# Kernel tuning notes

Hardware: AMD Instinct MI355X
Metric: run time of the kernel (lower is better)

The kernel has to match this reference:

```python
import jax, jax.numpy as jnp
import numpy as np

H = 4096          # hidden_size
M = 4096          # num tokens
BLK = 128         # fp8 quant group/block size
EPS = 1e-6
FP8_MAX = 448.0   # float8_e4m3fn max


def fp8_round(x):
    # round-trip through fp8 e4m3 to emulate FP8 storage
    return x.astype(jnp.float8_e4m3fn).astype(jnp.float32)


def rms_norm(x, w, eps=EPS):
    var = jnp.mean(x * x, axis=-1, keepdims=True)
    return x * jax.lax.rsqrt(var + eps) * w


def block_fp8_linear(x, w, wscale):
    # per-token group-128 activation quant + 128x128 block-scaled fp8 GEMM
    m, k = x.shape
    kb = k // BLK
    nb = w.shape[1] // BLK
    xr = x.reshape(m, kb, BLK)
    amax = jnp.max(jnp.abs(xr), axis=-1)                      # [m, kb]
    s = jnp.maximum(amax, 1e-12) / FP8_MAX                    # group scales
    q = fp8_round(xr / s[..., None])                          # fp8 values
    xdq = (q * s[..., None]).reshape(m, k)                    # dequant acts
    # dequantize weight blockwise: w already fp8-valued floats
    wdq = (w.reshape(kb, BLK, nb, BLK) * wscale[:, None, :, None]).reshape(k, nb * BLK)
    return xdq @ wdq


def setup_inputs() -> dict:
    key = jax.random.key(0)
    ks = jax.random.split(key, 8)
    x = jax.random.normal(ks[0], (M, H), dtype=jnp.float32)
    sb = H // BLK
    d = {"x": x}
    for i in range(3):
        w = fp8_round(jax.random.uniform(ks[1 + i], (H, H), dtype=jnp.float32)).T
        d[f"w{i}"] = w
        d[f"ws{i}"] = jax.random.uniform(ks[4 + i], (sb, sb), dtype=jnp.float32)
    for i in range(4):
        d[f"nw{i}"] = jnp.ones((H,), dtype=jnp.float32)
    return d


def reference(x, w0, ws0, w1, ws1, w2, ws2, nw0, nw1, nw2, nw3):
    x = jax.nn.relu(x)
    resid = x
    y = rms_norm(x, nw0)
    x2 = block_fp8_linear(y, w0, ws0)
    resid = x2 + resid
    y2 = rms_norm(resid, nw1)
    x3 = block_fp8_linear(y2, w1, ws1)
    resid = x3 + resid
    y3 = rms_norm(resid, nw2)
    x4 = block_fp8_linear(y3, w2, ws2)
    resid = x4 + resid
    y4 = rms_norm(resid, nw3)
    return y4
```

## Files before the change

kernel.cpp:

```cpp
#include <hip/hip_runtime.h>
#include <stdint.h>

#define H 4096

typedef float v4f __attribute__((ext_vector_type(4)));
typedef long long i64;
typedef long long v2l __attribute__((ext_vector_type(2)));

__device__ __forceinline__ void gload16(const uint8_t* g, uint8_t* l) {
  __builtin_amdgcn_global_load_lds(
      (const __attribute__((address_space(1))) uint8_t*)g,
      (__attribute__((address_space(3))) uint8_t*)l, 16, 0, 0);
}

__device__ __forceinline__ int permpos(int kg) {
  const int kb = kg >> 7, b = kg & 127;
  const int ks = b >> 5, q = (b >> 3) & 3, j = b & 7;
  return kb * 128 + q * 32 + ks * 8 + j;
}

__global__ __launch_bounds__(256) void conv_w_kernel(
    const float* __restrict__ w0, const float* __restrict__ w1,
    const float* __restrict__ w2, uint8_t* __restrict__ o0,
    uint8_t* __restrict__ o1, uint8_t* __restrict__ o2) {
  const float* w = (blockIdx.z == 0) ? w0 : (blockIdx.z == 1 ? w1 : w2);
  uint8_t* o = (blockIdx.z == 0) ? o0 : (blockIdx.z == 1 ? o1 : o2);
  __shared__ uint8_t t[64][68];
  const int tid = threadIdx.x;
  const int k0 = blockIdx.y * 64, n0 = blockIdx.x * 64;
  const int rr = tid >> 4, cc = (tid & 15) * 4;
#pragma unroll
  for (int j = 0; j < 4; ++j) {
    const int r = rr + j * 16;
    v4f f = *(const v4f*)(w + (size_t)(k0 + r) * H + n0 + cc);
    unsigned p = __builtin_amdgcn_cvt_pk_fp8_f32(f.x, f.y, 0, false);
    p = __builtin_amdgcn_cvt_pk_fp8_f32(f.z, f.w, p, true);
    t[cc + 0][r] = p & 0xff;
    t[cc + 1][r] = (p >> 8) & 0xff;
    t[cc + 2][r] = (p >> 16) & 0xff;
    t[cc + 3][r] = p >> 24;
  }
  __syncthreads();
#pragma unroll
  for (int j = 0; j < 4; ++j) {
    const int n = rr + j * 16;
    unsigned p = (unsigned)t[n][cc] | ((unsigned)t[n][cc + 1] << 8) |
                 ((unsigned)t[n][cc + 2] << 16) |
                 ((unsigned)t[n][cc + 3] << 24);
    *(unsigned*)(o + (size_t)(n0 + n) * H + permpos(k0 + cc)) = p;
  }
}

__global__ __launch_bounds__(256) void quant_kernel(
    const float* in, const float* __restrict__ nw, uint8_t* __restrict__ q,
    float* __restrict__ sxT, const int relu) {
  const int row = blockIdx.x, tid = threadIdx.x;
  const v4f* rp = (const v4f*)(in + (size_t)row * H);
  v4f v[4];
  float ss = 0.f;
#pragma unroll
  for (int j = 0; j < 4; ++j) {
    v4f x = rp[j * 256 + tid];
    if (relu) {
      x.x = fmaxf(x.x, 0.f); x.y = fmaxf(x.y, 0.f);
      x.z = fmaxf(x.z, 0.f); x.w = fmaxf(x.w, 0.f);
    }
    v[j] = x;
    ss += x.x * x.x + x.y * x.y + x.z * x.z + x.w * x.w;
  }
#pragma unroll
  for (int o = 32; o > 0; o >>= 1) ss += __shfl_down(ss, o);
  __shared__ float red[4];
  if ((tid & 63) == 0) red[tid >> 6] = ss;
  __syncthreads();
  ss = red[0] + red[1] + red[2] + red[3];
  const float rinv = 1.f / sqrtf(ss * (1.f / H) + 1e-6f);
#pragma unroll
  for (int j = 0; j < 4; ++j) {
    v4f nv = ((const v4f*)nw)[j * 256 + tid];
    v4f y;
    y.x = v[j].x * rinv * nv.x;
    y.y = v[j].y * rinv * nv.y;
    y.z = v[j].z * rinv * nv.z;
    y.w = v[j].w * rinv * nv.w;
    float am = fmaxf(fmaxf(fabsf(y.x), fabsf(y.y)), fmaxf(fabsf(y.z), fabsf(y.w)));
#pragma unroll
    for (int o = 16; o > 0; o >>= 1) am = fmaxf(am, __shfl_xor(am, o, 32));
    const float s = fmaxf(am, 1e-12f) / 448.f;
    unsigned p = __builtin_amdgcn_cvt_pk_fp8_f32(y.x / s, y.y / s, 0, false);
    p = __builtin_amdgcn_cvt_pk_fp8_f32(y.z / s, y.w / s, p, true);
    const int col = (j * 256 + tid) * 4;
    *(unsigned*)(q + (size_t)row * H + permpos(col)) = p;
    if ((tid & 31) == 0)
      sxT[(size_t)(j * 8 + (tid >> 5)) * 4096 + row] = s;
  }
}

__global__ __launch_bounds__(256) void norm_kernel(float* io,
                                                   const float* __restrict__ nw) {
  const int row = blockIdx.x, tid = threadIdx.x;
  v4f* rp = (v4f*)(io + (size_t)row * H);
  v4f v[4];
  float ss = 0.f;
#pragma unroll
  for (int j = 0; j < 4; ++j) {
    v4f x = rp[j * 256 + tid];
    v[j] = x;
    ss += x.x * x.x + x.y * x.y + x.z * x.z + x.w * x.w;
  }
#pragma unroll
  for (int o = 32; o > 0; o >>= 1) ss += __shfl_down(ss, o);
  __shared__ float red[4];
  if ((tid & 63) == 0) red[tid >> 6] = ss;
  __syncthreads();
  ss = red[0] + red[1] + red[2] + red[3];
  const float rinv = 1.f / sqrtf(ss * (1.f / H) + 1e-6f);
#pragma unroll
  for (int j = 0; j < 4; ++j) {
    v4f nv = ((const v4f*)nw)[j * 256 + tid];
    v4f y;
    y.x = v[j].x * rinv * nv.x;
    y.y = v[j].y * rinv * nv.y;
    y.z = v[j].z * rinv * nv.z;
    y.w = v[j].w * rinv * nv.w;
    rp[j * 256 + tid] = y;
  }
}

__global__ __launch_bounds__(256, 4) void gemm_kernel(
    const uint8_t* __restrict__ qa,
    const float* __restrict__ sxT,
    const uint8_t* __restrict__ wt,
    const float* __restrict__ ws,
    const float* resid, float* outp, const int relu) {
  __shared__ __attribute__((aligned(16))) uint8_t sA[16384];
  __shared__ __attribute__((aligned(16))) uint8_t sB[16384];
  __shared__ __attribute__((aligned(16))) float scb[128];
  __shared__ float ws_s[32];

  const int tid = threadIdx.x;
  const int n0 = blockIdx.x * 128, m0 = blockIdx.y * 128;
  if (tid < 32) ws_s[tid] = ws[tid * 32 + blockIdx.x];

  const int wv = tid >> 6, lane = tid & 63;
  const int quad = lane >> 4, l16 = lane & 15;
  const int wm = wv >> 1, wn = wv & 1;

  const int swc = (tid & 7) ^ ((tid >> 3) & 7);
  const uint8_t* gA = qa + (size_t)(m0 + (tid >> 3)) * H + swc * 16;
  const uint8_t* gB = wt + (size_t)(n0 + (tid >> 3)) * H + swc * 16;
  const uint8_t* gS = (const uint8_t*)sxT + (size_t)m0 * 4 + lane * 16;
  uint8_t* lA = sA + wv * 1024;
  uint8_t* lB = sB + wv * 1024;

  int offp[2];
#pragma unroll
  for (int ksp = 0; ksp < 2; ++ksp)
    offp[ksp] = (((quad * 2 + ksp) ^ (l16 & 7)) << 4);
  const int arow = (wm * 64 + l16) * 128;
  const int brow = (wn * 64 + l16) * 128;
  const int scoff = wm * 64 + quad * 4;

  const v4f zf = {0.f, 0.f, 0.f, 0.f};
  v4f acc[4][4];
#pragma unroll
  for (int i = 0; i < 4; ++i)
#pragma unroll
    for (int j = 0; j < 4; ++j) acc[i][j] = zf;

  for (int kb = 0; kb < 32; ++kb) {
#pragma unroll
    for (int i = 0; i < 4; ++i) {
      gload16(gA + (size_t)i * (32 * H), lA + i * 4096);
      gload16(gB + (size_t)i * (32 * H), lB + i * 4096);
    }
    if (wv == 0 && lane < 32) gload16(gS + (size_t)kb * 16384, (uint8_t*)scb);
    gA += 128;
    gB += 128;
    __syncthreads();

    const float wsk = ws_s[kb];
    v2l bf[4][2];
#pragma unroll
    for (int tc = 0; tc < 4; ++tc)
#pragma unroll
      for (int ksp = 0; ksp < 2; ++ksp)
        bf[tc][ksp] = *(const v2l*)(sB + brow + tc * 2048 + offp[ksp]);

#pragma unroll
    for (int tr = 0; tr < 4; ++tr) {
      const v2l a0 = *(const v2l*)(sA + arow + tr * 2048 + offp[0]);
      const v2l a1 = *(const v2l*)(sA + arow + tr * 2048 + offp[1]);
      const v4f s4 = *(const v4f*)(scb + scoff + tr * 16) * wsk;
#pragma unroll
      for (int tc = 0; tc < 4; ++tc) {
        v4f p = __builtin_amdgcn_mfma_f32_16x16x32_fp8_fp8(a0.x, bf[tc][0].x, zf, 0, 0, 0);
        p = __builtin_amdgcn_mfma_f32_16x16x32_fp8_fp8(a0.y, bf[tc][0].y, p, 0, 0, 0);
        p = __builtin_amdgcn_mfma_f32_16x16x32_fp8_fp8(a1.x, bf[tc][1].x, p, 0, 0, 0);
        p = __builtin_amdgcn_mfma_f32_16x16x32_fp8_fp8(a1.y, bf[tc][1].y, p, 0, 0, 0);
        acc[tr][tc] += p * s4;
      }
    }
    __syncthreads();
  }

  const int mB = m0 + wm * 64 + quad * 4;
  const int nB = n0 + wn * 64 + l16;
#pragma unroll
  for (int tr = 0; tr < 4; ++tr) {
#pragma unroll
    for (int r = 0; r < 4; ++r) {
      const size_t rowOff = (size_t)(mB + tr * 16 + r) * H;
#pragma unroll
      for (int tc = 0; tc < 4; ++tc) {
        const size_t idx = rowOff + nB + tc * 16;
        float rv = resid[idx];
        if (relu) rv = fmaxf(rv, 0.f);
        outp[idx] = acc[tr][tc][r] + rv;
      }
    }
  }
}

extern "C" void kernel_launch(void* const* d_in, const int* in_sizes, int n_in,
                              void* d_out, int out_size, void* d_ws, size_t ws_size,
                              hipStream_t stream) {
  const float* x   = (const float*)d_in[0];
  const float* w0  = (const float*)d_in[1];
  const float* ws0 = (const float*)d_in[2];
  const float* w1  = (const float*)d_in[3];
  const float* ws1 = (const float*)d_in[4];
  const float* w2  = (const float*)d_in[5];
  const float* ws2 = (const float*)d_in[6];
  const float* nw0 = (const float*)d_in[7];
  const float* nw1 = (const float*)d_in[8];
  const float* nw2 = (const float*)d_in[9];
  const float* nw3 = (const float*)d_in[10];
  float* R = (float*)d_out;

  uint8_t* base = (uint8_t*)d_ws;
  uint8_t* wq0 = base;
  uint8_t* wq1 = base + ((size_t)16 << 20);
  uint8_t* wq2 = base + ((size_t)32 << 20);
  uint8_t* qa  = base + ((size_t)48 << 20);
  float* sa    = (float*)(base + ((size_t)64 << 20));

  conv_w_kernel<<<dim3(64, 64, 3), 256, 0, stream>>>(w0, w1, w2, wq0, wq1, wq2);

  quant_kernel<<<4096, 256, 0, stream>>>(x, nw0, qa, sa, 1);
  gemm_kernel<<<dim3(32, 32), 256, 0, stream>>>(qa, sa, wq0, ws0, x, R, 1);

  quant_kernel<<<4096, 256, 0, stream>>>(R, nw1, qa, sa, 0);
  gemm_kernel<<<dim3(32, 32), 256, 0, stream>>>(qa, sa, wq1, ws1, R, R, 0);

  quant_kernel<<<4096, 256, 0, stream>>>(R, nw2, qa, sa, 0);
  gemm_kernel<<<dim3(32, 32), 256, 0, stream>>>(qa, sa, wq2, ws2, R, R, 0);

  norm_kernel<<<4096, 256, 0, stream>>>(R, nw3);
}
```

Measured before the change: 686.7 us.

## Enlarge GEMM tile to 256x256 with double-buffered LDS prefetch

The block-scaled FP8 GEMM moves from 128x128 tiles with 256 threads to 256x256 tiles with 512 threads. LDS is double-buffered, and the next K-block's global-to-LDS loads are issued in four phases interleaved with the MFMA work. Block IDs are remapped so neighbouring blocks share A/B panels in L2, and s_setprio is raised around the MFMA sections. The aim is to cut per-tile global traffic and hide load latency behind compute. In exchange there are 256 blocks over 256 CUs (about one wave), much more LDS (about 130KB) and more accumulator registers.

After: 771.2 us. +12.3%, slower.

```diff
diff --git a/kernel.cpp b/kernel.cpp
--- a/kernel.cpp
+++ b/kernel.cpp
@@ -127,87 +127,120 @@
   }
 }
 
-__global__ __launch_bounds__(256, 4) void gemm_kernel(
+__global__ __launch_bounds__(512, 2) void gemm_kernel(
     const uint8_t* __restrict__ qa,
     const float* __restrict__ sxT,
     const uint8_t* __restrict__ wt,
     const float* __restrict__ ws,
     const float* resid, float* outp, const int relu) {
-  __shared__ __attribute__((aligned(16))) uint8_t sA[16384];
-  __shared__ __attribute__((aligned(16))) uint8_t sB[16384];
-  __shared__ __attribute__((aligned(16))) float scb[128];
-  __shared__ float ws_s[32];
+  __shared__ __attribute__((aligned(16))) uint8_t sA[2][32768];
+  __shared__ __attribute__((aligned(16))) uint8_t sB[2][32768];
+  __shared__ __attribute__((aligned(16))) float scb[2][256];
+  __shared__ float ws_s[64];
 
   const int tid = threadIdx.x;
-  const int n0 = blockIdx.x * 128, m0 = blockIdx.y * 128;
-  if (tid < 32) ws_s[tid] = ws[tid * 32 + blockIdx.x];
-
-  const int wv = tid >> 6, lane = tid & 63;
+
+  const int lid = blockIdx.y * 16 + blockIdx.x;
+  const int nl = (lid & 7) * 32 + (lid >> 3);
+  const int m0 = (nl >> 4) * 256, n0 = (nl & 15) * 256;
+
+  const int w = tid >> 6, lane = tid & 63;
   const int quad = lane >> 4, l16 = lane & 15;
-  const int wm = wv >> 1, wn = wv & 1;
-
-  const int swc = (tid & 7) ^ ((tid >> 3) & 7);
-  const uint8_t* gA = qa + (size_t)(m0 + (tid >> 3)) * H + swc * 16;
-  const uint8_t* gB = wt + (size_t)(n0 + (tid >> 3)) * H + swc * 16;
+  const int wm = w >> 2, wn = w & 3;
+  const int whalf = wn >> 1;
+
+  if (tid < 64) ws_s[tid] = ws[(tid >> 1) * 32 + (n0 >> 7) + (tid & 1)];
+
+  const int sw = (tid & 7) ^ ((tid >> 3) & 7);
+  const uint8_t* gA = qa + (size_t)(m0 + (tid >> 3)) * H + sw * 16;
+  const uint8_t* gB = wt + (size_t)(n0 + (tid >> 3)) * H + sw * 16;
   const uint8_t* gS = (const uint8_t*)sxT + (size_t)m0 * 4 + lane * 16;
-  uint8_t* lA = sA + wv * 1024;
-  uint8_t* lB = sB + wv * 1024;
+  const int ldst = w * 1024;
+
+#pragma unroll
+  for (int i = 0; i < 4; ++i) {
+    gload16(gA + (size_t)i * (64 * H), sA[0] + i * 8192 + ldst);
+    gload16(gB + (size_t)i * (64 * H), sB[0] + i * 8192 + ldst);
+  }
+  if (w == 0) gload16(gS, (uint8_t*)scb[0]);
 
   int offp[2];
 #pragma unroll
   for (int ksp = 0; ksp < 2; ++ksp)
     offp[ksp] = (((quad * 2 + ksp) ^ (l16 & 7)) << 4);
-  const int arow = (wm * 64 + l16) * 128;
-  const int brow = (wn * 64 + l16) * 128;
-  const int scoff = wm * 64 + quad * 4;
 
   const v4f zf = {0.f, 0.f, 0.f, 0.f};
-  v4f acc[4][4];
-#pragma unroll
-  for (int i = 0; i < 4; ++i)
+  v4f acc[8][4];
+#pragma unroll
+  for (int i = 0; i < 8; ++i)
 #pragma unroll
     for (int j = 0; j < 4; ++j) acc[i][j] = zf;
 
+  __syncthreads();
+
   for (int kb = 0; kb < 32; ++kb) {
-#pragma unroll
-    for (int i = 0; i < 4; ++i) {
-      gload16(gA + (size_t)i * (32 * H), lA + i * 4096);
-      gload16(gB + (size_t)i * (32 * H), lB + i * 4096);
+    const int cur = kb & 1, nxt = cur ^ 1;
+    const uint8_t* Ab = sA[cur];
+    const uint8_t* Bb = sB[cur];
+    const float* sc = scb[cur];
+    const float wsk = ws_s[kb * 2 + whalf];
+    const bool pf = (kb < 31);
+    v2l bf[4][2];
+
+#pragma unroll
+    for (int p = 0; p < 4; ++p) {
+      if (p == 0) {
+#pragma unroll
+        for (int tc = 0; tc < 4; ++tc)
+#pragma unroll
+          for (int ksp = 0; ksp < 2; ++ksp)
+            bf[tc][ksp] =
+                *(const v2l*)(Bb + (wn * 64 + tc * 16 + l16) * 128 + offp[ksp]);
+      }
+      v2l a[2][2];
+      v4f s4[2];
+#pragma unroll
+      for (int t = 0; t < 2; ++t) {
+        const int row = wm * 128 + (p * 2 + t) * 16 + l16;
+        a[t][0] = *(const v2l*)(Ab + row * 128 + offp[0]);
+        a[t][1] = *(const v2l*)(Ab + row * 128 + offp[1]);
+        s4[t] = *(const v4f*)(sc + wm * 128 + (p * 2 + t) * 16 + quad * 4);
+      }
+      if (pf) {
+        gload16(gA + 128 + (size_t)p * (64 * H), sA[nxt] + p * 8192 + ldst);
+        gload16(gB + 128 + (size_t)p * (64 * H), sB[nxt] + p * 8192 + ldst);
+        if (p == 0 && w == 0) gload16(gS + 16384, (uint8_t*)scb[nxt]);
+      }
+      __builtin_amdgcn_s_barrier();
+      asm volatile("s_waitcnt lgkmcnt(0)" ::: "memory");
+      __builtin_amdgcn_sched_barrier(0);
+      __builtin_amdgcn_s_setprio(1);
+#pragma unroll
+      for (int t = 0; t < 2; ++t) {
+        const int tr = p * 2 + t;
+        const v4f sv = s4[t] * wsk;
+#pragma unroll
+        for (int tc = 0; tc < 4; ++tc) {
+          v4f pr = __builtin_amdgcn_mfma_f32_16x16x32_fp8_fp8(a[t][0].x, bf[tc][0].x, zf, 0, 0, 0);
+          pr = __builtin_amdgcn_mfma_f32_16x16x32_fp8_fp8(a[t][0].y, bf[tc][0].y, pr, 0, 0, 0);
+          pr = __builtin_amdgcn_mfma_f32_16x16x32_fp8_fp8(a[t][1].x, bf[tc][1].x, pr, 0, 0, 0);
+          pr = __builtin_amdgcn_mfma_f32_16x16x32_fp8_fp8(a[t][1].y, bf[tc][1].y, pr, 0, 0, 0);
+          acc[tr][tc] += pr * sv;
+        }
+      }
+      __builtin_amdgcn_s_setprio(0);
+      if (p == 3) asm volatile("s_waitcnt vmcnt(0)" ::: "memory");
+      __builtin_amdgcn_s_barrier();
     }
-    if (wv == 0 && lane < 32) gload16(gS + (size_t)kb * 16384, (uint8_t*)scb);
     gA += 128;
     gB += 128;
-    __syncthreads();
-
-    const float wsk = ws_s[kb];
-    v2l bf[4][2];
-#pragma unroll
-    for (int tc = 0; tc < 4; ++tc)
-#pragma unroll
-      for (int ksp = 0; ksp < 2; ++ksp)
-        bf[tc][ksp] = *(const v2l*)(sB + brow + tc * 2048 + offp[ksp]);
-
-#pragma unroll
-    for (int tr = 0; tr < 4; ++tr) {
-      const v2l a0 = *(const v2l*)(sA + arow + tr * 2048 + offp[0]);
-      const v2l a1 = *(const v2l*)(sA + arow + tr * 2048 + offp[1]);
-      const v4f s4 = *(const v4f*)(scb + scoff + tr * 16) * wsk;
-#pragma unroll
-      for (int tc = 0; tc < 4; ++tc) {
-        v4f p = __builtin_amdgcn_mfma_f32_16x16x32_fp8_fp8(a0.x, bf[tc][0].x, zf, 0, 0, 0);
-        p = __builtin_amdgcn_mfma_f32_16x16x32_fp8_fp8(a0.y, bf[tc][0].y, p, 0, 0, 0);
-        p = __builtin_amdgcn_mfma_f32_16x16x32_fp8_fp8(a1.x, bf[tc][1].x, p, 0, 0, 0);
-        p = __builtin_amdgcn_mfma_f32_16x16x32_fp8_fp8(a1.y, bf[tc][1].y, p, 0, 0, 0);
-        acc[tr][tc] += p * s4;
-      }
-    }
-    __syncthreads();
-  }
-
-  const int mB = m0 + wm * 64 + quad * 4;
+    gS += 16384;
+  }
+
+  const int mB = m0 + wm * 128 + quad * 4;
   const int nB = n0 + wn * 64 + l16;
 #pragma unroll
-  for (int tr = 0; tr < 4; ++tr) {
+  for (int tr = 0; tr < 8; ++tr) {
 #pragma unroll
     for (int r = 0; r < 4; ++r) {
       const size_t rowOff = (size_t)(mB + tr * 16 + r) * H;
@@ -248,13 +281,13 @@
   conv_w_kernel<<<dim3(64, 64, 3), 256, 0, stream>>>(w0, w1, w2, wq0, wq1, wq2);
 
   quant_kernel<<<4096, 256, 0, stream>>>(x, nw0, qa, sa, 1);
-  gemm_kernel<<<dim3(32, 32), 256, 0, stream>>>(qa, sa, wq0, ws0, x, R, 1);
+  gemm_kernel<<<dim3(16, 16), 512, 0, stream>>>(qa, sa, wq0, ws0, x, R, 1);
 
   quant_kernel<<<4096, 256, 0, stream>>>(R, nw1, qa, sa, 0);
-  gemm_kernel<<<dim3(32, 32), 256, 0, stream>>>(qa, sa, wq1, ws1, R, R, 0);
+  gemm_kernel<<<dim3(16, 16), 512, 0, stream>>>(qa, sa, wq1, ws1, R, R, 0);
 
   quant_kernel<<<4096, 256, 0, stream>>>(R, nw2, qa, sa, 0);
-  gemm_kernel<<<dim3(32, 32), 256, 0, stream>>>(qa, sa, wq2, ws2, R, R, 0);
+  gemm_kernel<<<dim3(16, 16), 512, 0, stream>>>(qa, sa, wq2, ws2, R, R, 0);
 
   norm_kernel<<<4096, 256, 0, stream>>>(R, nw3);
 }
```
